# Performance work log

Measured on AMD Instinct MI355X. Metric: run time of the kernel, lower is better.

The kernel has to match this reference:

```python
import jax, jax.numpy as jnp
import numpy as np


def _patchify(x, p):
    # x: [B, V, H, W] -> [B, V, L, p*p] with L = (H/p)*(W/p), matching Conv2d(kernel=stride=p)
    B, V, H, W = x.shape
    hp, wp = H // p, W // p
    x = x.reshape(B, V, hp, p, wp, p)
    x = x.transpose(0, 1, 2, 4, 3, 5)  # [B, V, hp, wp, p, p]
    return x.reshape(B, V, hp * wp, p * p)


def setup_inputs() -> dict:
    key = jax.random.key(0)
    ks = jax.random.split(key, 12)
    B, V, H, W, p, D = 2, 16, 128, 256, 4, 1024
    L = (H // p) * (W // p)  # 2048
    std = 0.02
    return {
        "x": jax.random.normal(ks[0], (B, V, H, W), jnp.float32),
        "proj_w": jax.random.normal(ks[1], (V, D, p * p), jnp.float32) * std,
        "proj_b": jnp.zeros((V, D), jnp.float32),
        "channel_embed": jax.random.normal(ks[2], (1, V, D), jnp.float32) * std,
        "pos_embed": jax.random.normal(ks[3], (1, L, D), jnp.float32) * std,
        "channel_query": jax.random.normal(ks[4], (1, 1, D), jnp.float32) * std,
        "wq": jax.random.normal(ks[5], (D, D), jnp.float32) * std,
        "wk": jax.random.normal(ks[6], (D, D), jnp.float32) * std,
        "wv": jax.random.normal(ks[7], (D, D), jnp.float32) * std,
        "bq": jnp.zeros((D,), jnp.float32),
        "bk": jnp.zeros((D,), jnp.float32),
        "bv": jnp.zeros((D,), jnp.float32),
        "wo": jax.random.normal(ks[8], (D, D), jnp.float32) * std,
        "bo": jnp.zeros((D,), jnp.float32),
        "num_heads": 16,
    }


def reference(x, proj_w, proj_b, channel_embed, pos_embed, channel_query,
              wq, wk, wv, bq, bk, bv, wo, bo, num_heads):
    D = proj_w.shape[1]
    p = int(round(np.sqrt(proj_w.shape[-1])))
    nh = int(num_heads)
    dh = D // nh

    # per-variable patch embed (Conv2d k=stride=p == patch-matmul)
    patches = _patchify(x, p)                                   # [B, V, L, p*p]
    tok = jnp.einsum('bvlk,vdk->bvld', patches, proj_w)         # [B, V, L, D]
    tok = tok + proj_b[None, :, None, :]

    # add variable (channel) and positional embeddings
    tok = tok + channel_embed[:, :, None, :] + pos_embed[:, None, :, :]

    # aggregate_variables: single-query MHA over V, batched over B*L
    h = tok.transpose(0, 2, 1, 3)                               # [B, L, V, D]
    q = channel_query[0, 0] @ wq.T + bq                         # [D]
    qh = q.reshape(nh, dh)
    k = (jnp.einsum('blvd,ed->blve', h, wk) + bk).reshape(*h.shape[:3], nh, dh)
    v = (jnp.einsum('blvd,ed->blve', h, wv) + bv).reshape(*h.shape[:3], nh, dh)
    scores = jnp.einsum('he,blvhe->blhv', qh, k) / np.sqrt(dh)  # [B, L, nh, V]
    attn = jax.nn.softmax(scores, axis=-1)
    ctx = jnp.einsum('blhv,blvhe->blhe', attn, v)               # [B, L, nh, dh]
    ctx = ctx.reshape(h.shape[0], h.shape[1], D)
    out = ctx @ wo.T + bo                                       # [B, L, D]
    return out
```

## Files before the change

### kernel.cpp

```cpp
#include <hip/hip_runtime.h>
#include <hip/hip_bf16.h>

using bf16 = __hip_bfloat16;
using bf16x8 = __attribute__((ext_vector_type(8))) short;
using f32x4  = __attribute__((ext_vector_type(4))) float;

__device__ inline unsigned short f2bu(float f){ bf16 h = __float2bfloat16(f); return *(unsigned short*)&h; }
__device__ inline void async_cp16(const void* g, void* l){
  __builtin_amdgcn_global_load_lds((const __attribute__((address_space(1))) void*)g,
                                   (__attribute__((address_space(3))) void*)l, 16, 0, 0);
}
union BF8 { unsigned short s[8]; bf16x8 v; };

constexpr int D_ = 1024, L_ = 2048;
constexpr int CN = 384;

__global__ __launch_bounds__(256) void k_prep(const float* __restrict__ wv, const float* __restrict__ wo,
                                              const float* __restrict__ pe, const float* __restrict__ proj_w,
                                              const float* __restrict__ proj_b, const float* __restrict__ ce,
                                              const float* __restrict__ cq, const float* __restrict__ wq,
                                              const float* __restrict__ bq,
                                              unsigned short* __restrict__ Ab, unsigned short* __restrict__ wo_b,
                                              unsigned short* __restrict__ peb, unsigned short* __restrict__ Btb,
                                              float* __restrict__ q){
  __shared__ float t[64][17];
  const int blk = blockIdx.x;
  const int tid = threadIdx.x;
  if (blk < 4096){
    int i = blk*256 + tid;
    const float* src; unsigned short* dst; size_t off;
    if (i < 262144)      { src = wv; dst = Ab;   off = i; }
    else if (i < 524288) { src = wo; dst = wo_b; off = i - 262144; }
    else                 { src = pe; dst = peb;  off = i - 524288; }
    float4 v = *(const float4*)(src + off*4);
    *(ushort4*)(dst + off*4) = make_ushort4(f2bu(v.x), f2bu(v.y), f2bu(v.z), f2bu(v.w));
  } else if (blk < 4352){
    const int r_ = blk - 4096;
    const int v = r_ >> 4, dd0 = (r_ & 15)*64;
    { const int r = tid >> 2, kq = tid & 3;
      float4 a = *(const float4*)(proj_w + ((size_t)(v*D_ + dd0 + r))*16 + kq*4);
      t[r][kq*4+0]=a.x; t[r][kq*4+1]=a.y; t[r][kq*4+2]=a.z; t[r][kq*4+3]=a.w; }
    __syncthreads();
    { const int k = tid >> 4, c0 = (tid & 15)*4;
      ushort4 o = make_ushort4(f2bu(t[c0+0][k]), f2bu(t[c0+1][k]), f2bu(t[c0+2][k]), f2bu(t[c0+3][k]));
      *(ushort4*)(Btb + (size_t)(v*16+k)*D_ + dd0 + c0) = o; }
    if (tid < 16){
      const int c0 = tid*4;
      float4 pb = *(const float4*)(proj_b + v*D_ + dd0 + c0);
      float4 cc = *(const float4*)(ce     + v*D_ + dd0 + c0);
      ushort4 o = make_ushort4(f2bu(pb.x+cc.x), f2bu(pb.y+cc.y), f2bu(pb.z+cc.z), f2bu(pb.w+cc.w));
      *(ushort4*)(Btb + (size_t)(256+v)*D_ + dd0 + c0) = o;
    }
  } else {
    const int bq_ = blk - 4352;
    const int wave = tid >> 6, lane = tid & 63;
    float cqv[16];
    #pragma unroll
    for (int k=0;k<16;++k) cqv[k] = cq[lane + 64*k];
    #pragma unroll
    for (int j=0;j<16;++j){
      const int e = bq_*64 + wave*16 + j;
      const float* wr = wq + (size_t)e*D_;
      float p = 0.f;
      #pragma unroll
      for (int k=0;k<16;++k) p += cqv[k]*wr[lane + 64*k];
      #pragma unroll
      for (int m=32;m>=1;m>>=1) p += __shfl_xor(p, m, 64);
      if (lane==0) q[e] = p + bq[e];
    }
  }
}

__global__ __launch_bounds__(256) void k_qwk3(const float* __restrict__ q, const float* __restrict__ wk,
                                              unsigned short* __restrict__ Abq){
  __shared__ float red[4][64];
  const int hh = blockIdx.x >> 4, dq = blockIdx.x & 15;
  const int eg = threadIdx.x >> 6, dl = threadIdx.x & 63;
  const int d = dq*64 + dl;
  float s = 0.f;
  #pragma unroll
  for (int j=0;j<16;++j){
    int e = hh*64 + eg*16 + j;
    s += q[e]*wk[(size_t)e*D_ + d];
  }
  red[eg][dl] = s;
  __syncthreads();
  if (eg==0)
    Abq[(size_t)hh*D_ + d] = f2bu(((red[0][dl]+red[1][dl]) + (red[2][dl]+red[3][dl]))*0.125f);
}

__device__ inline void gemm64_body(unsigned short* As, unsigned short* Bs,
                                   const unsigned short* __restrict__ A, const unsigned short* __restrict__ Bt,
                                   float* __restrict__ C, unsigned short* __restrict__ W,
                                   int m0, int n0, int K, int ldc, int Mvalid){
  const int tid = threadIdx.x;
  const int wave = tid >> 6, lane = tid & 63;
  const int wm = wave & 1, wn = wave >> 1;
  const int lm = lane & 15, kg4 = lane >> 4;
  f32x4 acc[2][4];
  #pragma unroll
  for (int mf=0;mf<2;++mf)
    #pragma unroll
    for (int nf=0;nf<4;++nf) acc[mf][nf] = (f32x4){0.f,0.f,0.f,0.f};
  for (int k0=0; k0<K; k0+=64){
    #pragma unroll
    for (int i=0;i<2;++i){
      int idx = i*256 + tid;
      int row = idx >> 3, g = (idx & 7) ^ (row & 7);
      async_cp16(A + (size_t)(m0+row)*K + k0 + g*8, &As[idx*8]);
    }
    #pragma unroll
    for (int i=0;i<4;++i){
      int idx = i*256 + tid;
      int row = idx >> 3, g = (idx & 7) ^ (row & 7);
      async_cp16(Bt + (size_t)(n0+row)*K + k0 + g*8, &Bs[idx*8]);
    }
    __syncthreads();
    #pragma unroll
    for (int c=0;c<2;++c){
      bf16x8 af[2], bfr[4];
      #pragma unroll
      for (int f=0;f<2;++f){
        int row = wm*32 + f*16 + lm;
        af[f] = *(const bf16x8*)(&As[row*64 + (((c*4+kg4) ^ (row&7)))*8]);
      }
      #pragma unroll
      for (int f=0;f<4;++f){
        int colr = wn*64 + f*16 + lm;
        bfr[f] = *(const bf16x8*)(&Bs[colr*64 + (((c*4+kg4) ^ (colr&7)))*8]);
      }
      #pragma unroll
      for (int mf=0;mf<2;++mf)
        #pragma unroll
        for (int nf=0;nf<4;++nf)
          acc[mf][nf] = __builtin_amdgcn_mfma_f32_16x16x32_bf16(af[mf], bfr[nf], acc[mf][nf], 0,0,0);
    }
    __syncthreads();
  }
  #pragma unroll
  for (int nf=0;nf<4;++nf){
    int col = n0 + wn*64 + nf*16 + lm;
    #pragma unroll
    for (int mf=0;mf<2;++mf){
      #pragma unroll
      for (int r=0;r<4;++r){
        int row = m0 + wm*32 + mf*16 + kg4*4 + r;
        if (row < Mvalid){
          float v = acc[mf][nf][r];
          C[(size_t)row*ldc + col] = v;
          if (row < 1024 && col < 256) W[(size_t)row*256 + col] = f2bu(v);
        }
      }
    }
  }
}

template<bool BIAS>
__device__ inline void gemm128_body(unsigned short* As, unsigned short* Bs,
                                    const unsigned short* __restrict__ A, const unsigned short* __restrict__ Bt,
                                    const float* __restrict__ bias, float* __restrict__ C,
                                    int m0, int n0, int K, int ldc){
  const int tid = threadIdx.x;
  const int wave = tid >> 6, lane = tid & 63;
  const int wm = wave & 1, wn = wave >> 1;
  const int lm = lane & 15, kg4 = lane >> 4;
  f32x4 acc[4][4];
  #pragma unroll
  for (int mf=0;mf<4;++mf)
    #pragma unroll
    for (int nf=0;nf<4;++nf) acc[mf][nf] = (f32x4){0.f,0.f,0.f,0.f};
  for (int k0=0; k0<K; k0+=64){
    #pragma unroll
    for (int i=0;i<4;++i){
      int idx = i*256 + tid;
      int row = idx >> 3, g = (idx & 7) ^ (row & 7);
      async_cp16(A + (size_t)(m0+row)*K + k0 + g*8, &As[idx*8]);
    }
    #pragma unroll
    for (int i=0;i<4;++i){
      int idx = i*256 + tid;
      int row = idx >> 3, g = (idx & 7) ^ (row & 7);
      async_cp16(Bt + (size_t)(n0+row)*K + k0 + g*8, &Bs[idx*8]);
    }
    __syncthreads();
    #pragma unroll
    for (int c=0;c<2;++c){
      bf16x8 af[4], bfr[4];
      #pragma unroll
      for (int f=0;f<4;++f){
        int row = wm*64 + f*16 + lm;
        af[f] = *(const bf16x8*)(&As[row*64 + (((c*4+kg4) ^ (row&7)))*8]);
      }
      #pragma unroll
      for (int f=0;f<4;++f){
        int colr = wn*64 + f*16 + lm;
        bfr[f] = *(const bf16x8*)(&Bs[colr*64 + (((c*4+kg4) ^ (colr&7)))*8]);
      }
      #pragma unroll
      for (int mf=0;mf<4;++mf)
        #pragma unroll
        for (int nf=0;nf<4;++nf)
          acc[mf][nf] = __builtin_amdgcn_mfma_f32_16x16x32_bf16(af[mf], bfr[nf], acc[mf][nf], 0,0,0);
    }
    __syncthreads();
  }
  #pragma unroll
  for (int nf=0;nf<4;++nf){
    int col = n0 + wn*64 + nf*16 + lm;
    float bval = BIAS ? bias[col] : 0.f;
    #pragma unroll
    for (int mf=0;mf<4;++mf){
      #pragma unroll
      for (int r=0;r<4;++r){
        int row = m0 + wm*64 + mf*16 + kg4*4 + r;
        C[(size_t)row*ldc + col] = acc[mf][nf][r] + bval;
      }
    }
  }
}

__global__ __launch_bounds__(256) void k_gemmCP(const unsigned short* __restrict__ Ab,
                                                const unsigned short* __restrict__ Btb,
                                                const unsigned short* __restrict__ peb,
                                                float* __restrict__ Cbig, unsigned short* __restrict__ Wb2,
                                                float* __restrict__ P2){
  __shared__ unsigned short As[128*64];
  __shared__ unsigned short Bs[128*64];
  if (blockIdx.x < 51){
    int bx = blockIdx.x % 3, by = blockIdx.x / 3;
    gemm64_body(As, Bs, Ab, Btb, Cbig, Wb2, by*64, bx*128, 1024, CN, 1040);
  } else {
    int b = blockIdx.x - 51;
    int bx = b & 7, by = b >> 3;
    gemm128_body<false>(As, Bs, peb, Ab, nullptr, P2, by*128, bx*128, 1024, 1024);
  }
}

__global__ __launch_bounds__(256) void k_gemmOut(const unsigned short* __restrict__ ctxF,
                                                 const unsigned short* __restrict__ wo_b,
                                                 const float* __restrict__ bo, float* __restrict__ C){
  __shared__ unsigned short As[128*64];
  __shared__ unsigned short Bs[128*64];
  gemm128_body<true>(As, Bs, ctxF, wo_b, bo, C, blockIdx.y*128, blockIdx.x*128, 1024, 1024);
}

__global__ __launch_bounds__(256) void k_fused6(const float* __restrict__ x,
                                                const float* __restrict__ Cbig,
                                                const unsigned short* __restrict__ Wb2,
                                                const float* __restrict__ bv,
                                                const float* __restrict__ P2,
                                                unsigned short* __restrict__ ctxF){
  __shared__ float patchP[16*260];
  __shared__ float attnT[8*320];
  const int tid = threadIdx.x;
  const int bb = blockIdx.x >> 8;
  const int sg = (blockIdx.x >> 1) & 127;
  const int hq = blockIdx.x & 1;
  unsigned short* ctx = ctxF + (size_t)bb*L_*D_;
  {
    const int s = tid >> 4, v = tid & 15;
    const int l = sg*16 + s;
    const int hi = l >> 6, wi = l & 63;
    const float* xp = x + ((size_t)((bb*16+v)*128 + hi*4)*256 + wi*4);
    float* dst = &patchP[s*260 + v*16];
    #pragma unroll
    for (int pi=0; pi<4; ++pi){
      float4 r = *(const float4*)(xp + pi*256);
      dst[pi*4+0]=r.x; dst[pi*4+1]=r.y; dst[pi*4+2]=r.z; dst[pi*4+3]=r.w;
    }
  }
  __syncthreads();
  if (tid < 128){
    const int s = tid >> 3, h8 = tid & 7;
    const int hh = hq*8 + h8;
    const float* qrow = Cbig + (size_t)(1024+hh)*CN;
    const float* prow = &patchP[s*260];
    float sc[16];
    #pragma unroll
    for (int v=0; v<16; ++v){
      float a = qrow[256+v];
      const float* qp = qrow + v*16;
      const float* pp = prow + v*16;
      #pragma unroll
      for (int k=0;k<16;++k) a += qp[k]*pp[k];
      sc[v] = a;
    }
    float mx = sc[0];
    #pragma unroll
    for (int v=1;v<16;++v) mx = fmaxf(mx, sc[v]);
    float sum = 0.f;
    #pragma unroll
    for (int v=0;v<16;++v){ sc[v] = __expf(sc[v]-mx); sum += sc[v]; }
    float inv = 1.f/sum;
    float* arow = &attnT[h8*320 + s*20];
    #pragma unroll
    for (int v=0;v<16;++v) arow[v] = sc[v]*inv;
  }
  __syncthreads();
  const int wave = tid >> 6, lane = tid & 63;
  const int m = lane & 15, quad = lane >> 4;
  const int l0 = sg*16;
  #pragma unroll
  for (int it=0; it<2; ++it){
    const int h8 = wave*2 + it;
    const int hh = hq*8 + h8;
    const float* at = &attnT[h8*320];
    f32x4 acc[4];
    #pragma unroll
    for (int dt=0;dt<4;++dt) acc[dt] = (f32x4){0.f,0.f,0.f,0.f};
    #pragma unroll
    for (int vp=0; vp<8; ++vp){
      const int v = vp*2 + (quad>>1);
      const int k8 = (quad&1)*8;
      const float aw = at[m*20 + v];
      const float* pp = &patchP[m*260 + v*16 + k8];
      BF8 af;
      #pragma unroll
      for (int j=0;j<8;++j) af.s[j] = f2bu(aw*pp[j]);
      #pragma unroll
      for (int dt=0; dt<4; ++dt){
        const int d = hh*64 + dt*16 + m;
        const bf16x8 bf = *(const bf16x8*)(Wb2 + (size_t)d*256 + vp*32 + quad*8);
        acc[dt] = __builtin_amdgcn_mfma_f32_16x16x32_bf16(af.v, bf, acc[dt], 0,0,0);
      }
    }
    #pragma unroll
    for (int dt=0; dt<4; ++dt){
      const int d = hh*64 + dt*16 + m;
      const float* c0p = Cbig + (size_t)d*CN + 256;
      float c0v[16];
      #pragma unroll
      for (int j=0;j<4;++j){
        float4 t = *(const float4*)(c0p + 4*j);
        c0v[4*j+0]=t.x; c0v[4*j+1]=t.y; c0v[4*j+2]=t.z; c0v[4*j+3]=t.w;
      }
      const float bvd = bv[d];
      #pragma unroll
      for (int r=0;r<4;++r){
        const int s = quad*4 + r;
        float dot = bvd;
        const float* as_ = at + s*20;
        #pragma unroll
        for (int v=0;v<16;++v) dot += as_[v]*c0v[v];
        ctx[(size_t)(l0+s)*D_ + d] = f2bu(acc[dt][r] + dot + P2[(size_t)(l0+s)*D_ + d]);
      }
    }
  }
}

extern "C" void kernel_launch(void* const* d_in, const int* in_sizes, int n_in,
                              void* d_out, int out_size, void* d_ws, size_t ws_size,
                              hipStream_t stream){
  const float* x      = (const float*)d_in[0];
  const float* proj_w = (const float*)d_in[1];
  const float* proj_b = (const float*)d_in[2];
  const float* ce     = (const float*)d_in[3];
  const float* pe     = (const float*)d_in[4];
  const float* cq     = (const float*)d_in[5];
  const float* wq     = (const float*)d_in[6];
  const float* wk     = (const float*)d_in[7];
  const float* wv     = (const float*)d_in[8];
  const float* bq     = (const float*)d_in[9];
  const float* bv     = (const float*)d_in[11];
  const float* wo     = (const float*)d_in[12];
  const float* bo     = (const float*)d_in[13];
  float* out = (float*)d_out;

  char* base = (char*)d_ws;
  float*          q    = (float*)(base);
  unsigned short* Ab   = (unsigned short*)(base + 4096);
  unsigned short* Btb  = (unsigned short*)(base + 2363392);
  float*          Cbig = (float*)(base + 3149824);
  unsigned short* wo_b = (unsigned short*)(base + 4747264);
  unsigned short* Wb2  = (unsigned short*)(base + 6844416);
  unsigned short* peb  = (unsigned short*)(base + 7368704);
  float*          P2   = (float*)(base + 11563008);
  unsigned short* ctxF = (unsigned short*)(base + 19951616);

  k_prep<<<4368, 256, 0, stream>>>(wv, wo, pe, proj_w, proj_b, ce, cq, wq, bq,
                                   Ab, wo_b, peb, Btb, q);
  k_qwk3<<<256, 256, 0, stream>>>(q, wk, Ab + (size_t)1024*D_);
  k_gemmCP<<<179, 256, 0, stream>>>(Ab, Btb, peb, Cbig, Wb2, P2);
  k_fused6<<<512, 256, 0, stream>>>(x, Cbig, Wb2, bv, P2, ctxF);
  k_gemmOut<<<dim3(8,32), 256, 0, stream>>>(ctxF, wo_b, bo, out);
}
```

Measured before the change: 195.3 us.

## Fold positional-embedding V path into output GEMM via precomposed Wo·Wv weight

Result: faster. 190.7 us (-2.3%).

```diff
diff --git a/kernel.cpp b/kernel.cpp
--- a/kernel.cpp
+++ b/kernel.cpp
@@ -15,15 +15,18 @@
 constexpr int D_ = 1024, L_ = 2048;
 constexpr int CN = 384;
 
-__global__ __launch_bounds__(256) void k_prep(const float* __restrict__ wv, const float* __restrict__ wo,
-                                              const float* __restrict__ pe, const float* __restrict__ proj_w,
-                                              const float* __restrict__ proj_b, const float* __restrict__ ce,
-                                              const float* __restrict__ cq, const float* __restrict__ wq,
-                                              const float* __restrict__ bq,
-                                              unsigned short* __restrict__ Ab, unsigned short* __restrict__ wo_b,
-                                              unsigned short* __restrict__ peb, unsigned short* __restrict__ Btb,
-                                              float* __restrict__ q){
-  __shared__ float t[64][17];
+__global__ __launch_bounds__(256) void k_prep3(const float* __restrict__ wv, const float* __restrict__ wo,
+                                               const float* __restrict__ pe, const float* __restrict__ proj_w,
+                                               const float* __restrict__ proj_b, const float* __restrict__ ce,
+                                               const float* __restrict__ cq, const float* __restrict__ wq,
+                                               const float* __restrict__ bq, const float* __restrict__ wk,
+                                               unsigned short* __restrict__ Ab, unsigned short* __restrict__ wo_b,
+                                               unsigned short* __restrict__ peb, unsigned short* __restrict__ Btb,
+                                               unsigned short* __restrict__ wvTb){
+  __shared__ float t68[64][68];
+  __shared__ float t17[64][17];
+  __shared__ float qL[64];
+  __shared__ float red[4][64];
   const int blk = blockIdx.x;
   const int tid = threadIdx.x;
   if (blk < 4096){
@@ -39,10 +42,10 @@
     const int v = r_ >> 4, dd0 = (r_ & 15)*64;
     { const int r = tid >> 2, kq = tid & 3;
       float4 a = *(const float4*)(proj_w + ((size_t)(v*D_ + dd0 + r))*16 + kq*4);
-      t[r][kq*4+0]=a.x; t[r][kq*4+1]=a.y; t[r][kq*4+2]=a.z; t[r][kq*4+3]=a.w; }
+      t17[r][kq*4+0]=a.x; t17[r][kq*4+1]=a.y; t17[r][kq*4+2]=a.z; t17[r][kq*4+3]=a.w; }
     __syncthreads();
     { const int k = tid >> 4, c0 = (tid & 15)*4;
-      ushort4 o = make_ushort4(f2bu(t[c0+0][k]), f2bu(t[c0+1][k]), f2bu(t[c0+2][k]), f2bu(t[c0+3][k]));
+      ushort4 o = make_ushort4(f2bu(t17[c0+0][k]), f2bu(t17[c0+1][k]), f2bu(t17[c0+2][k]), f2bu(t17[c0+3][k]));
       *(ushort4*)(Btb + (size_t)(v*16+k)*D_ + dd0 + c0) = o; }
     if (tid < 16){
       const int c0 = tid*4;
@@ -51,48 +54,66 @@
       ushort4 o = make_ushort4(f2bu(pb.x+cc.x), f2bu(pb.y+cc.y), f2bu(pb.z+cc.z), f2bu(pb.w+cc.w));
       *(ushort4*)(Btb + (size_t)(256+v)*D_ + dd0 + c0) = o;
     }
+  } else if (blk < 4608){
+    const int r2 = blk - 4352;
+    const int d0 = (r2 >> 4)*64, dd0 = (r2 & 15)*64;
+    const int r = tid >> 2, c0 = (tid & 3)*16;
+    #pragma unroll
+    for (int j=0;j<4;++j){
+      float4 v = *(const float4*)(wv + (size_t)(d0+r)*D_ + dd0 + c0 + 4*j);
+      t68[r][c0+4*j+0] = v.x; t68[r][c0+4*j+1] = v.y; t68[r][c0+4*j+2] = v.z; t68[r][c0+4*j+3] = v.w;
+    }
+    __syncthreads();
+    #pragma unroll
+    for (int j=0;j<4;++j){
+      ushort4 o = make_ushort4(f2bu(t68[c0+4*j+0][r]), f2bu(t68[c0+4*j+1][r]),
+                               f2bu(t68[c0+4*j+2][r]), f2bu(t68[c0+4*j+3][r]));
+      *(ushort4*)(wvTb + (size_t)(dd0+r)*D_ + d0 + c0 + 4*j) = o;
+    }
   } else {
-    const int bq_ = blk - 4352;
+    const int b = blk - 4608;
+    const int hh = b >> 4, dq = b & 15;
     const int wave = tid >> 6, lane = tid & 63;
-    float cqv[16];
-    #pragma unroll
-    for (int k=0;k<16;++k) cqv[k] = cq[lane + 64*k];
-    #pragma unroll
-    for (int j=0;j<16;++j){
-      const int e = bq_*64 + wave*16 + j;
-      const float* wr = wq + (size_t)e*D_;
-      float p = 0.f;
-      #pragma unroll
-      for (int k=0;k<16;++k) p += cqv[k]*wr[lane + 64*k];
-      #pragma unroll
-      for (int m=32;m>=1;m>>=1) p += __shfl_xor(p, m, 64);
-      if (lane==0) q[e] = p + bq[e];
-    }
-  }
-}
-
-__global__ __launch_bounds__(256) void k_qwk3(const float* __restrict__ q, const float* __restrict__ wk,
-                                              unsigned short* __restrict__ Abq){
-  __shared__ float red[4][64];
-  const int hh = blockIdx.x >> 4, dq = blockIdx.x & 15;
-  const int eg = threadIdx.x >> 6, dl = threadIdx.x & 63;
-  const int d = dq*64 + dl;
-  float s = 0.f;
-  #pragma unroll
-  for (int j=0;j<16;++j){
-    int e = hh*64 + eg*16 + j;
-    s += q[e]*wk[(size_t)e*D_ + d];
-  }
-  red[eg][dl] = s;
-  __syncthreads();
-  if (eg==0)
-    Abq[(size_t)hh*D_ + d] = f2bu(((red[0][dl]+red[1][dl]) + (red[2][dl]+red[3][dl]))*0.125f);
-}
-
-__device__ inline void gemm64_body(unsigned short* As, unsigned short* Bs,
-                                   const unsigned short* __restrict__ A, const unsigned short* __restrict__ Bt,
-                                   float* __restrict__ C, unsigned short* __restrict__ W,
-                                   int m0, int n0, int K, int ldc, int Mvalid){
+    {
+      float cqv[16];
+      #pragma unroll
+      for (int k=0;k<16;++k) cqv[k] = cq[lane + 64*k];
+      #pragma unroll
+      for (int j=0;j<16;++j){
+        const int e = hh*64 + wave*16 + j;
+        const float* wr = wq + (size_t)e*D_;
+        float p = 0.f;
+        #pragma unroll
+        for (int k=0;k<16;++k) p += cqv[k]*wr[lane + 64*k];
+        #pragma unroll
+        for (int m=32;m>=1;m>>=1) p += __shfl_xor(p, m, 64);
+        if (lane==0) qL[wave*16+j] = p + bq[e];
+      }
+    }
+    __syncthreads();
+    {
+      const int eg = wave, dl = lane;
+      const int d = dq*64 + dl;
+      float s = 0.f;
+      #pragma unroll
+      for (int j=0;j<16;++j){
+        int e = hh*64 + eg*16 + j;
+        s += qL[eg*16+j]*wk[(size_t)e*D_ + d];
+      }
+      red[eg][dl] = s;
+      __syncthreads();
+      if (eg==0)
+        Ab[(size_t)(1024+hh)*D_ + d] = f2bu(((red[0][dl]+red[1][dl]) + (red[2][dl]+red[3][dl]))*0.125f);
+    }
+  }
+}
+
+template<bool BIAS, bool WB2, bool BOUT>
+__device__ inline void gemm64_body3(unsigned short* As, unsigned short* Bs,
+                                    const unsigned short* __restrict__ A, const unsigned short* __restrict__ Bt,
+                                    const float* __restrict__ bias, float* __restrict__ C,
+                                    unsigned short* __restrict__ W,
+                                    int m0, int n0, int K, int ldc, int Mvalid){
   const int tid = threadIdx.x;
   const int wave = tid >> 6, lane = tid & 63;
   const int wm = wave & 1, wn = wave >> 1;
@@ -140,6 +161,7 @@
   #pragma unroll
   for (int nf=0;nf<4;++nf){
     int col = n0 + wn*64 + nf*16 + lm;
+    float bval = BIAS ? bias[col] : 0.f;
     #pragma unroll
     for (int mf=0;mf<2;++mf){
       #pragma unroll
@@ -147,48 +169,78 @@
         int row = m0 + wm*32 + mf*16 + kg4*4 + r;
         if (row < Mvalid){
           float v = acc[mf][nf][r];
-          C[(size_t)row*ldc + col] = v;
-          if (row < 1024 && col < 256) W[(size_t)row*256 + col] = f2bu(v);
+          if (BOUT){
+            W[(size_t)row*ldc + col] = f2bu(v);
+          } else {
+            C[(size_t)row*ldc + col] = v + bval;
+            if (WB2 && row < 1024 && col < 256) W[(size_t)row*256 + col] = f2bu(v);
+          }
         }
       }
     }
   }
 }
 
-template<bool BIAS>
-__device__ inline void gemm128_body(unsigned short* As, unsigned short* Bs,
-                                    const unsigned short* __restrict__ A, const unsigned short* __restrict__ Bt,
-                                    const float* __restrict__ bias, float* __restrict__ C,
-                                    int m0, int n0, int K, int ldc){
+__global__ __launch_bounds__(256) void k_gemmCW(const unsigned short* __restrict__ Ab,
+                                                const unsigned short* __restrict__ Btb,
+                                                const unsigned short* __restrict__ wo_b,
+                                                const unsigned short* __restrict__ wvTb,
+                                                float* __restrict__ Cbig, unsigned short* __restrict__ Wb2,
+                                                unsigned short* __restrict__ W2b){
+  __shared__ unsigned short As[64*64];
+  __shared__ unsigned short Bs[128*64];
+  if (blockIdx.x < 51){
+    int bx = blockIdx.x % 3, by = blockIdx.x / 3;
+    gemm64_body3<false,true,false>(As, Bs, Ab, Btb, nullptr, Cbig, Wb2, by*64, bx*128, 1024, CN, 1040);
+  } else {
+    int b = blockIdx.x - 51;
+    int bx = b & 7, by = b >> 3;
+    gemm64_body3<false,false,true>(As, Bs, wo_b, wvTb, nullptr, nullptr, W2b, by*64, bx*128, 1024, 1024, 1024);
+  }
+}
+
+__global__ __launch_bounds__(256) void k_gemmOutCat(const unsigned short* __restrict__ ctxF,
+                                                    const unsigned short* __restrict__ wo_b,
+                                                    const unsigned short* __restrict__ peb,
+                                                    const unsigned short* __restrict__ W2b,
+                                                    const float* __restrict__ bo, float* __restrict__ C){
+  __shared__ unsigned short As[64*64];
+  __shared__ unsigned short Bs[128*64];
   const int tid = threadIdx.x;
   const int wave = tid >> 6, lane = tid & 63;
   const int wm = wave & 1, wn = wave >> 1;
+  const int m0 = blockIdx.y*64, n0 = blockIdx.x*128;
   const int lm = lane & 15, kg4 = lane >> 4;
-  f32x4 acc[4][4];
+  f32x4 acc[2][4];
   #pragma unroll
-  for (int mf=0;mf<4;++mf)
+  for (int mf=0;mf<2;++mf)
     #pragma unroll
     for (int nf=0;nf<4;++nf) acc[mf][nf] = (f32x4){0.f,0.f,0.f,0.f};
-  for (int k0=0; k0<K; k0+=64){
+  for (int k0=0; k0<2048; k0+=64){
+    const bool first = (k0 < 1024);
+    const int kk = first ? k0 : (k0 - 1024);
+    #pragma unroll
+    for (int i=0;i<2;++i){
+      int idx = i*256 + tid;
+      int row = idx >> 3, g = (idx & 7) ^ (row & 7);
+      const unsigned short* ap = first ? (ctxF + (size_t)(m0+row)*1024)
+                                       : (peb + (size_t)((m0+row)&2047)*1024);
+      async_cp16(ap + kk + g*8, &As[idx*8]);
+    }
     #pragma unroll
     for (int i=0;i<4;++i){
       int idx = i*256 + tid;
       int row = idx >> 3, g = (idx & 7) ^ (row & 7);
-      async_cp16(A + (size_t)(m0+row)*K + k0 + g*8, &As[idx*8]);
-    }
-    #pragma unroll
-    for (int i=0;i<4;++i){
-      int idx = i*256 + tid;
-      int row = idx >> 3, g = (idx & 7) ^ (row & 7);
-      async_cp16(Bt + (size_t)(n0+row)*K + k0 + g*8, &Bs[idx*8]);
+      const unsigned short* bp = first ? wo_b : W2b;
+      async_cp16(bp + (size_t)(n0+row)*1024 + kk + g*8, &Bs[idx*8]);
     }
     __syncthreads();
     #pragma unroll
     for (int c=0;c<2;++c){
-      bf16x8 af[4], bfr[4];
-      #pragma unroll
-      for (int f=0;f<4;++f){
-        int row = wm*64 + f*16 + lm;
+      bf16x8 af[2], bfr[4];
+      #pragma unroll
+      for (int f=0;f<2;++f){
+        int row = wm*32 + f*16 + lm;
         af[f] = *(const bf16x8*)(&As[row*64 + (((c*4+kg4) ^ (row&7)))*8]);
       }
       #pragma unroll
@@ -197,7 +249,7 @@
         bfr[f] = *(const bf16x8*)(&Bs[colr*64 + (((c*4+kg4) ^ (colr&7)))*8]);
       }
       #pragma unroll
-      for (int mf=0;mf<4;++mf)
+      for (int mf=0;mf<2;++mf)
         #pragma unroll
         for (int nf=0;nf<4;++nf)
           acc[mf][nf] = __builtin_amdgcn_mfma_f32_16x16x32_bf16(af[mf], bfr[nf], acc[mf][nf], 0,0,0);
@@ -207,48 +259,22 @@
   #pragma unroll
   for (int nf=0;nf<4;++nf){
     int col = n0 + wn*64 + nf*16 + lm;
-    float bval = BIAS ? bias[col] : 0.f;
-    #pragma unroll
-    for (int mf=0;mf<4;++mf){
+    float bval = bo[col];
+    #pragma unroll
+    for (int mf=0;mf<2;++mf){
       #pragma unroll
       for (int r=0;r<4;++r){
-        int row = m0 + wm*64 + mf*16 + kg4*4 + r;
-        C[(size_t)row*ldc + col] = acc[mf][nf][r] + bval;
-      }
-    }
-  }
-}
-
-__global__ __launch_bounds__(256) void k_gemmCP(const unsigned short* __restrict__ Ab,
-                                                const unsigned short* __restrict__ Btb,
-                                                const unsigned short* __restrict__ peb,
-                                                float* __restrict__ Cbig, unsigned short* __restrict__ Wb2,
-                                                float* __restrict__ P2){
-  __shared__ unsigned short As[128*64];
-  __shared__ unsigned short Bs[128*64];
-  if (blockIdx.x < 51){
-    int bx = blockIdx.x % 3, by = blockIdx.x / 3;
-    gemm64_body(As, Bs, Ab, Btb, Cbig, Wb2, by*64, bx*128, 1024, CN, 1040);
-  } else {
-    int b = blockIdx.x - 51;
-    int bx = b & 7, by = b >> 3;
-    gemm128_body<false>(As, Bs, peb, Ab, nullptr, P2, by*128, bx*128, 1024, 1024);
-  }
-}
-
-__global__ __launch_bounds__(256) void k_gemmOut(const unsigned short* __restrict__ ctxF,
-                                                 const unsigned short* __restrict__ wo_b,
-                                                 const float* __restrict__ bo, float* __restrict__ C){
-  __shared__ unsigned short As[128*64];
-  __shared__ unsigned short Bs[128*64];
-  gemm128_body<true>(As, Bs, ctxF, wo_b, bo, C, blockIdx.y*128, blockIdx.x*128, 1024, 1024);
-}
-
-__global__ __launch_bounds__(256) void k_fused6(const float* __restrict__ x,
+        int row = m0 + wm*32 + mf*16 + kg4*4 + r;
+        C[(size_t)row*1024 + col] = acc[mf][nf][r] + bval;
+      }
+    }
+  }
+}
+
+__global__ __launch_bounds__(256) void k_fused8(const float* __restrict__ x,
                                                 const float* __restrict__ Cbig,
                                                 const unsigned short* __restrict__ Wb2,
                                                 const float* __restrict__ bv,
-                                                const float* __restrict__ P2,
                                                 unsigned short* __restrict__ ctxF){
   __shared__ float patchP[16*260];
   __shared__ float attnT[8*320];
@@ -257,12 +283,12 @@
   const int sg = (blockIdx.x >> 1) & 127;
   const int hq = blockIdx.x & 1;
   unsigned short* ctx = ctxF + (size_t)bb*L_*D_;
+  const int l0 = sg*16;
   {
-    const int s = tid >> 4, v = tid & 15;
-    const int l = sg*16 + s;
-    const int hi = l >> 6, wi = l & 63;
-    const float* xp = x + ((size_t)((bb*16+v)*128 + hi*4)*256 + wi*4);
-    float* dst = &patchP[s*260 + v*16];
+    const int v = tid >> 4, u = tid & 15;
+    const int hi = l0 >> 6, wi0 = l0 & 63;
+    const float* xp = x + ((size_t)((bb*16+v)*128 + hi*4)*256 + (wi0+u)*4);
+    float* dst = &patchP[u*260 + v*16];
     #pragma unroll
     for (int pi=0; pi<4; ++pi){
       float4 r = *(const float4*)(xp + pi*256);
@@ -299,7 +325,6 @@
   __syncthreads();
   const int wave = tid >> 6, lane = tid & 63;
   const int m = lane & 15, quad = lane >> 4;
-  const int l0 = sg*16;
   #pragma unroll
   for (int it=0; it<2; ++it){
     const int h8 = wave*2 + it;
@@ -342,7 +367,7 @@
         const float* as_ = at + s*20;
         #pragma unroll
         for (int v=0;v<16;++v) dot += as_[v]*c0v[v];
-        ctx[(size_t)(l0+s)*D_ + d] = f2bu(acc[dt][r] + dot + P2[(size_t)(l0+s)*D_ + d]);
+        ctx[(size_t)(l0+s)*D_ + d] = f2bu(acc[dt][r] + dot);
       }
     }
   }
@@ -367,20 +392,19 @@
   float* out = (float*)d_out;
 
   char* base = (char*)d_ws;
-  float*          q    = (float*)(base);
-  unsigned short* Ab   = (unsigned short*)(base + 4096);
-  unsigned short* Btb  = (unsigned short*)(base + 2363392);
-  float*          Cbig = (float*)(base + 3149824);
-  unsigned short* wo_b = (unsigned short*)(base + 4747264);
-  unsigned short* Wb2  = (unsigned short*)(base + 6844416);
-  unsigned short* peb  = (unsigned short*)(base + 7368704);
-  float*          P2   = (float*)(base + 11563008);
-  unsigned short* ctxF = (unsigned short*)(base + 19951616);
-
-  k_prep<<<4368, 256, 0, stream>>>(wv, wo, pe, proj_w, proj_b, ce, cq, wq, bq,
-                                   Ab, wo_b, peb, Btb, q);
-  k_qwk3<<<256, 256, 0, stream>>>(q, wk, Ab + (size_t)1024*D_);
-  k_gemmCP<<<179, 256, 0, stream>>>(Ab, Btb, peb, Cbig, Wb2, P2);
-  k_fused6<<<512, 256, 0, stream>>>(x, Cbig, Wb2, bv, P2, ctxF);
-  k_gemmOut<<<dim3(8,32), 256, 0, stream>>>(ctxF, wo_b, bo, out);
-}
+  unsigned short* Ab   = (unsigned short*)(base);
+  unsigned short* Btb  = (unsigned short*)(base + 2359296);
+  float*          Cbig = (float*)(base + 3145728);
+  unsigned short* wo_b = (unsigned short*)(base + 4743168);
+  unsigned short* Wb2  = (unsigned short*)(base + 6840320);
+  unsigned short* wvTb = (unsigned short*)(base + 7364608);
+  unsigned short* W2b  = (unsigned short*)(base + 9461760);
+  unsigned short* peb  = (unsigned short*)(base + 11558912);
+  unsigned short* ctxF = (unsigned short*)(base + 15753216);
+
+  k_prep3<<<4864, 256, 0, stream>>>(wv, wo, pe, proj_w, proj_b, ce, cq, wq, bq, wk,
+                                    Ab, wo_b, peb, Btb, wvTb);
+  k_gemmCW<<<179, 256, 0, stream>>>(Ab, Btb, wo_b, wvTb, Cbig, Wb2, W2b);
+  k_fused8<<<512, 256, 0, stream>>>(x, Cbig, Wb2, bv, ctxF);
+  k_gemmOutCat<<<dim3(8,64), 256, 0, stream>>>(ctxF, wo_b, peb, W2b, bo, out);
+}
```
